# Kernel tuning notes

Measured on AMD Instinct MI355X. Metric: run time of the kernel, lower is better.

The kernel has to match this reference:

```python
import jax, jax.numpy as jnp
import numpy as np

B, C, H, W = 2, 1024, 64, 64
E, TOP_K = 8, 2
FFN = C  # ffn_dim = in_channels; hidden_dim = out_channels = in_channels


def setup_inputs() -> dict:
    key = jax.random.key(0)
    ks = jax.random.split(key, 5)
    s = 0.02
    return {
        "hidden_states": jax.random.normal(ks[0], (B, C, H, W), jnp.float32),
        "gate_w": jax.random.normal(ks[1], (E, C), jnp.float32) * s,   # torch Linear weight [out,in]
        "w1": jax.random.normal(ks[2], (E, FFN, C), jnp.float32) * s,
        "w2": jax.random.normal(ks[3], (E, C, FFN), jnp.float32) * s,
        "w3": jax.random.normal(ks[4], (E, FFN, C), jnp.float32) * s,
    }


def reference(hidden_states, gate_w, w1, w2, w3):
    b, c = hidden_states.shape[0], hidden_states.shape[1]
    space = hidden_states.shape[2:]
    # (B, C, H, W) -> (B, H, W, C) -> (T, C)
    x = jnp.transpose(hidden_states, (0, 2, 3, 1)).reshape(-1, c)

    # Router: softmax in float32, top-k, renormalize (matches torch)
    logits = x @ gate_w.T                                   # [T, E]
    probs = jax.nn.softmax(logits.astype(jnp.float32), axis=-1)
    rw, sel = jax.lax.top_k(probs, TOP_K)                   # [T, K]
    rw = rw / jnp.sum(rw, axis=-1, keepdims=True)
    rw = rw.astype(x.dtype)

    # Combine weights per expert: zero where expert not selected -> exact
    # equivalence with gather/scatter dispatch (full capacity, no drops).
    combine = jnp.sum(jax.nn.one_hot(sel, E, dtype=x.dtype) * rw[..., None], axis=1)  # [T, E]

    out = jnp.zeros_like(x)
    for e in range(E):  # small fixed expert loop
        h = jax.nn.gelu(x @ w1[e].T, approximate=False) * (x @ w3[e].T)  # SwiGLU-style [T, FFN]
        out = out + combine[:, e:e + 1] * (h @ w2[e].T)

    out = out.reshape(b, *space, c)
    return jnp.transpose(out, (0, 3, 1, 2))  # (B, C, H, W)
```

## Files before the change

kernel.cpp:

```cpp
#include <hip/hip_runtime.h>
#include <hip/hip_bf16.h>
#include <math.h>

#define BB 2
#define CC 1024
#define HH 64
#define WW 64
#define HWH (HH*WW)
#define TT (BB*HWH)
#define EE 8
#define FFN 1024
#define MAXTILES 71
#define HCAP (MAXTILES*256)

typedef __bf16 bf16x8 __attribute__((ext_vector_type(8)));
typedef float  f32x4  __attribute__((ext_vector_type(4)));

__device__ __forceinline__ void gl_lds16(const __bf16* g, __bf16* l) {
    __builtin_amdgcn_global_load_lds(
        (const __attribute__((address_space(1))) void*)g,
        (__attribute__((address_space(3))) void*)l, 16, 0, 0);
}

__device__ __forceinline__ void barrier_raw() {
    asm volatile("" ::: "memory");
    __builtin_amdgcn_s_barrier();
    asm volatile("" ::: "memory");
}

#define WAITV(N) asm volatile("s_waitcnt vmcnt(" #N ")" ::: "memory")
#define LGKM0()  asm volatile("s_waitcnt lgkmcnt(0)" ::: "memory")
#define SCHED0() __builtin_amdgcn_sched_barrier(0)
#define PRIO1()  __builtin_amdgcn_s_setprio(1)
#define PRIO0()  __builtin_amdgcn_s_setprio(0)

#define CVB 12288
#define XPB 8192
#define RTB 512
__global__ __launch_bounds__(256) void k_prep(
    const float* __restrict__ hs, const float* __restrict__ gate_w,
    const float* __restrict__ w1, const float* __restrict__ w2,
    const float* __restrict__ w3,
    __bf16* __restrict__ w1b, __bf16* __restrict__ w2b,
    __bf16* __restrict__ w3b, __bf16* __restrict__ X,
    float* __restrict__ logP) {
    __shared__ float sm[2112];
    const int bid = blockIdx.x;
    const int tid = threadIdx.x;

    if (bid < CVB) {
        const float* s; __bf16* d; int lb = bid;
        if (lb < 4096)      { s = w1; d = w1b; }
        else if (lb < 8192) { s = w2; d = w2b; lb -= 4096; }
        else                { s = w3; d = w3b; lb -= 8192; }
        const size_t i = (size_t)lb * 2048 + (size_t)tid * 8;
        const f32x4 v0 = *(const f32x4*)&s[i];
        const f32x4 v1 = *(const f32x4*)&s[i + 4];
        bf16x8 o;
#pragma unroll
        for (int j = 0; j < 4; ++j) { o[j] = (__bf16)v0[j]; o[4 + j] = (__bf16)v1[j]; }
        *(bf16x8*)&d[i] = o;
    } else if (bid < CVB + XPB) {
        const int lb  = bid - CVB;
        const int hw0 = (lb & 127) * 32;
        const int c0  = ((lb >> 7) & 31) * 32;
        const int b   = lb >> 12;
        float (*tile)[33] = (float(*)[33])sm;
        const int tx = tid & 31, ty = tid >> 5;
        const float* src = hs + ((size_t)b * CC + c0) * HWH + hw0;
#pragma unroll
        for (int i = 0; i < 4; ++i)
            tile[ty + i * 8][tx] = src[(size_t)(ty + i * 8) * HWH + tx];
        __syncthreads();
        __bf16* dst = X + ((size_t)b * HWH + hw0) * CC + c0;
#pragma unroll
        for (int i = 0; i < 4; ++i) {
            const int hwl = ty + i * 8;
            dst[(size_t)hwl * CC + tx] = (__bf16)tile[tx][hwl];
        }
    } else {
        const int lb  = bid - (CVB + XPB);
        const int q   = lb & 3;
        const int t64 = lb >> 2;
        float* g = sm;
        for (int i = tid; i < 2048; i += 256)
            g[i] = gate_w[(size_t)(i >> 8) * CC + q * 256 + (i & 255)];
        __syncthreads();
        const int q2 = tid >> 6, tl = tid & 63;
        const int t  = t64 * 64 + tl;
        const int b  = t >> 12, hw = t & 4095;
        const float* xp = hs + (size_t)b * CC * HWH + hw;
        float l[EE];
#pragma unroll
        for (int e = 0; e < EE; ++e) l[e] = 0.0f;
        const int cbase = q * 256 + q2 * 64;
        for (int c2 = 0; c2 < 64; ++c2) {
            const float xv = xp[(size_t)(cbase + c2) * HWH];
#pragma unroll
            for (int e = 0; e < EE; ++e) l[e] += xv * g[e * 256 + q2 * 64 + c2];
        }
        float* dst = logP + ((size_t)(q * 4 + q2) * TT + t) * 8;
        f32x4 a, c;
#pragma unroll
        for (int e = 0; e < 4; ++e) { a[e] = l[e]; c[e] = l[4 + e]; }
        *(f32x4*)dst = a;
        *(f32x4*)&dst[4] = c;
    }
}

__global__ __launch_bounds__(256) void k_top2(const float* __restrict__ logP,
                                              int* __restrict__ cnt,
                                              int* __restrict__ idxl,
                                              int* __restrict__ tokE,
                                              int* __restrict__ tokP,
                                              float* __restrict__ tokW) {
    __shared__ int lcnt[EE], lbase[EE];
    const int tid = threadIdx.x;
    const int t   = blockIdx.x * 256 + tid;
    if (tid < EE) lcnt[tid] = 0;
    __syncthreads();

    float l[EE];
#pragma unroll
    for (int e = 0; e < EE; ++e) l[e] = 0.0f;
#pragma unroll
    for (int pq = 0; pq < 16; ++pq) {
        const float* src = logP + ((size_t)pq * TT + t) * 8;
        const f32x4 a = *(const f32x4*)src;
        const f32x4 c = *(const f32x4*)&src[4];
#pragma unroll
        for (int e = 0; e < 4; ++e) { l[e] += a[e]; l[4 + e] += c[e]; }
    }

    int e1 = 0; float v1 = l[0];
#pragma unroll
    for (int e = 1; e < EE; ++e) { if (l[e] > v1) { v1 = l[e]; e1 = e; } }
    int e2 = -1; float v2 = -1e30f;
#pragma unroll
    for (int e = 0; e < EE; ++e) { if (e != e1 && l[e] > v2) { v2 = l[e]; e2 = e; } }

    const float p2 = __expf(v2 - v1);
    const float rs = 1.0f / (1.0f + p2);

    const int m1 = atomicAdd(&lcnt[e1], 1);
    const int m2 = atomicAdd(&lcnt[e2], 1);
    __syncthreads();
    if (tid < EE) lbase[tid] = atomicAdd(&cnt[tid], lcnt[tid]);
    __syncthreads();
    const int p1pos = lbase[e1] + m1;
    const int p2pos = lbase[e2] + m2;

    idxl[e1 * TT + p1pos] = t;
    idxl[e2 * TT + p2pos] = t;
    tokE[t] = e1 | (e2 << 8);
    tokP[2 * t]     = p1pos;
    tokP[2 * t + 1] = p2pos;
    tokW[2 * t]     = rs;
    tokW[2 * t + 1] = p2 * rs;
}

__global__ void k_offsets(const int* __restrict__ cnt, int* __restrict__ off,
                          int* __restrict__ tileE, int* __restrict__ tileM,
                          int* __restrict__ nT) {
    if (threadIdx.x == 0) {
        int a = 0, n = 0;
        for (int e = 0; e < EE; ++e) {
            off[e] = a;
            const int mt = (cnt[e] + 255) >> 8;
            for (int m = 0; m < mt; ++m) { tileE[n] = e; tileM[n] = m * 256; ++n; }
            a += mt * 256;
        }
        nT[0] = n;
    }
}

__global__ __launch_bounds__(512, 1)
void k_gemm1(const __bf16* __restrict__ X, const __bf16* __restrict__ w1b,
             const __bf16* __restrict__ w3b, const int* __restrict__ cnt,
             const int* __restrict__ off, const int* __restrict__ idxl,
             const int* __restrict__ tileE, const int* __restrict__ tileM,
             const int* __restrict__ nT, __bf16* __restrict__ H) {
    if ((int)blockIdx.y >= nT[0]) return;
    const int e    = tileE[blockIdx.y];
    const int mt   = tileM[blockIdx.y];
    const int cntE = cnt[e];
    const int goff = off[e];
    const int n0   = blockIdx.x * 128;
    const __bf16* W1 = w1b + (size_t)e * FFN * CC;
    const __bf16* W3 = w3b + (size_t)e * FFN * CC;

    __shared__ __align__(16) __bf16 sA[2][2][256 * 32];
    __shared__ __align__(16) __bf16 sB[2][2][256 * 32];

    const int tid  = threadIdx.x;
    const int lane = tid & 63, wave = tid >> 6;
    const int l15  = lane & 15, lq = lane >> 4;
    const int wm   = wave & 1;
    const int q    = wave >> 1;
    const int rsw  = (lq ^ ((l15 >> 1) & 3)) * 8;

    const int rl  = lane >> 2;
    const int csw = ((lane & 3) ^ ((rl >> 1) & 3)) * 8;

    int pr0 = mt + wave * 32 + rl;       if (pr0 > cntE - 1) pr0 = cntE - 1;
    int pr1 = mt + wave * 32 + 16 + rl;  if (pr1 > cntE - 1) pr1 = cntE - 1;
    const __bf16* gA0 = X + (size_t)idxl[e * TT + pr0] * CC + csw;
    const __bf16* gA1 = X + (size_t)idxl[e * TT + pr1] * CC + csw;
    const __bf16* WB = (wave & 1) ? W3 : W1;
    const __bf16* gB0 = WB + (size_t)(n0 + q * 32 + rl) * CC + csw;
    const __bf16* gB1 = WB + (size_t)(n0 + q * 32 + 16 + rl) * CC + csw;

    const int st0  = wave * 1024;
    const int aoff = (wm * 128 + l15) * 32 + rsw;
    const int boff = (q * 64 + l15) * 32 + rsw;

    f32x4 acc[8][4] = {};

#define G1_STGA(S, KS, KB) do {                                               \
    gl_lds16(gA0 + (KB) + (KS) * 32, &sA[S][KS][st0]);                        \
    gl_lds16(gA1 + (KB) + (KS) * 32, &sA[S][KS][st0 + 512]); } while (0)
#define G1_STGB(S, KS, KB) do {                                               \
    gl_lds16(gB0 + (KB) + (KS) * 32, &sB[S][KS][st0]);                        \
    gl_lds16(gB1 + (KB) + (KS) * 32, &sB[S][KS][st0 + 512]); } while (0)
#define G1_LDA(DST, S, KS, MF0)                                               \
    _Pragma("unroll") for (int mf_ = 0; mf_ < 4; ++mf_)                       \
        DST[mf_] = *(const bf16x8*)&sA[S][KS][aoff + (MF0 + mf_) * 512];
#define G1_LDB(DST, S, KS)                                                    \
    _Pragma("unroll") for (int nf_ = 0; nf_ < 4; ++nf_)                       \
        DST[nf_] = *(const bf16x8*)&sB[S][KS][boff + nf_ * 512];
#define G1_MM(M0, AF, BF)                                                     \
    _Pragma("unroll") for (int m_ = 0; m_ < 4; ++m_)                          \
    _Pragma("unroll") for (int n_ = 0; n_ < 4; ++n_)                          \
        acc[M0 + m_][n_] = __builtin_amdgcn_mfma_f32_16x16x32_bf16(           \
            AF[m_], BF[n_], acc[M0 + m_][n_], 0, 0, 0);

#define G1_TILE(S, KB, STG, LAST) do {                                        \
    bf16x8 af[4], bv[4];                                                      \
                                 \
    G1_LDA(af, S, 0, 0); G1_LDB(bv, S, 0);                                    \
    if (STG) G1_STGA((S) ^ 1, 0, KB);                                         \
    barrier_raw(); LGKM0(); SCHED0();                                         \
    PRIO1(); G1_MM(0, af, bv); PRIO0(); barrier_raw();                        \
                                               \
    G1_LDA(af, S, 0, 4);                                                      \
    if (STG) G1_STGB((S) ^ 1, 0, KB);                                         \
    if (LAST) { WAITV(0); } else { WAITV(4); }                                \
    barrier_raw(); LGKM0(); SCHED0();                                         \
    PRIO1(); G1_MM(4, af, bv); PRIO0(); barrier_raw();                        \
                                 \
    G1_LDA(af, S, 1, 0); G1_LDB(bv, S, 1);                                    \
    if (STG) G1_STGA((S) ^ 1, 1, KB);                                         \
    barrier_raw(); LGKM0(); SCHED0();                                         \
    PRIO1(); G1_MM(0, af, bv); PRIO0(); barrier_raw();                        \
                                               \
    G1_LDA(af, S, 1, 4);                                                      \
    if (STG) G1_STGB((S) ^ 1, 1, KB);                                         \
    if (!LAST) { WAITV(4); }                                                  \
    barrier_raw(); LGKM0(); SCHED0();                                         \
    PRIO1(); G1_MM(4, af, bv); PRIO0(); barrier_raw();                        \
} while (0)

    G1_STGA(0, 0, 0); G1_STGB(0, 0, 0); G1_STGA(0, 1, 0); G1_STGB(0, 1, 0);
    WAITV(0);
    barrier_raw();

    int kb = 64;
    for (int it = 0; it < 7; ++it) {
        G1_TILE(0, kb, 1, 0); kb += 64;
        G1_TILE(1, kb, 1, 0); kb += 64;
    }
    G1_TILE(0, kb, 1, 0);
    G1_TILE(1, 0, 0, 1);

#undef G1_STGA
#undef G1_STGB
#undef G1_LDA
#undef G1_LDB
#undef G1_MM
#undef G1_TILE

#pragma unroll
    for (int mf = 0; mf < 8; ++mf) {
        const int gr = goff + mt + wm * 128 + mf * 16 + lq * 4;
#pragma unroll
        for (int jp = 0; jp < 2; ++jp) {
            const int col = n0 + q * 32 + jp * 16 + l15;
#pragma unroll
            for (int r = 0; r < 4; ++r) {
                const float a  = acc[mf][jp][r];
                const float c  = acc[mf][jp + 2][r];
                const float ge = 0.5f * a * (1.0f + erff(a * 0.70710678118654752f));
                H[(size_t)(gr + r) * FFN + col] = (__bf16)(ge * c);
            }
        }
    }
}

__global__ __launch_bounds__(512, 1)
void k_gemm2(const __bf16* __restrict__ H, const __bf16* __restrict__ w2b,
             const int* __restrict__ off, const int* __restrict__ tileE,
             const int* __restrict__ tileM, const int* __restrict__ nT,
             __bf16* __restrict__ Z) {
    if ((int)blockIdx.y >= nT[0]) return;
    const int e    = tileE[blockIdx.y];
    const int mt   = tileM[blockIdx.y];
    const int goff = off[e];
    const int n0   = blockIdx.x * 256;
    const __bf16* W2 = w2b + (size_t)e * CC * FFN;
    const __bf16* Ar = H + (size_t)(goff + mt) * FFN;

    __shared__ __align__(16) __bf16 sA[2][2][256 * 32];
    __shared__ __align__(16) __bf16 sB[2][2][256 * 32];

    const int tid  = threadIdx.x;
    const int lane = tid & 63, wave = tid >> 6;
    const int l15  = lane & 15, lq = lane >> 4;
    const int wm   = wave & 1;
    const int q    = wave >> 1;
    const int rsw  = (lq ^ ((l15 >> 1) & 3)) * 8;
    const int rl   = lane >> 2;
    const int csw  = ((lane & 3) ^ ((rl >> 1) & 3)) * 8;

    const __bf16* gA0 = Ar + (size_t)(wave * 32 + rl) * FFN + csw;
    const __bf16* gA1 = Ar + (size_t)(wave * 32 + 16 + rl) * FFN + csw;
    const __bf16* gB0 = W2 + (size_t)(n0 + wave * 32 + rl) * FFN + csw;
    const __bf16* gB1 = W2 + (size_t)(n0 + wave * 32 + 16 + rl) * FFN + csw;

    const int st0  = wave * 1024;
    const int aoff = (wm * 128 + l15) * 32 + rsw;
    const int boff = (q * 64 + l15) * 32 + rsw;

    f32x4 acc[8][4] = {};

#define G2_STGA(S, KS, KB) do {                                               \
    gl_lds16(gA0 + (KB) + (KS) * 32, &sA[S][KS][st0]);                        \
    gl_lds16(gA1 + (KB) + (KS) * 32, &sA[S][KS][st0 + 512]); } while (0)
#define G2_STGB(S, KS, KB) do {                                               \
    gl_lds16(gB0 + (KB) + (KS) * 32, &sB[S][KS][st0]);                        \
    gl_lds16(gB1 + (KB) + (KS) * 32, &sB[S][KS][st0 + 512]); } while (0)
#define G2_LDA(DST, S, KS, MF0)                                               \
    _Pragma("unroll") for (int mf_ = 0; mf_ < 4; ++mf_)                       \
        DST[mf_] = *(const bf16x8*)&sA[S][KS][aoff + (MF0 + mf_) * 512];
#define G2_LDB(DST, S, KS)                                                    \
    _Pragma("unroll") for (int nf_ = 0; nf_ < 4; ++nf_)                       \
        DST[nf_] = *(const bf16x8*)&sB[S][KS][boff + nf_ * 512];
#define G2_MM(M0, AF, BF)                                                     \
    _Pragma("unroll") for (int m_ = 0; m_ < 4; ++m_)                          \
    _Pragma("unroll") for (int n_ = 0; n_ < 4; ++n_)                          \
        acc[M0 + m_][n_] = __builtin_amdgcn_mfma_f32_16x16x32_bf16(           \
            AF[m_], BF[n_], acc[M0 + m_][n_], 0, 0, 0);

#define G2_TILE(S, KB, STG, LAST) do {                                        \
    bf16x8 af[4], bv[4];                                                      \
    G2_LDA(af, S, 0, 0); G2_LDB(bv, S, 0);                                    \
    if (STG) G2_STGA((S) ^ 1, 0, KB);                                         \
    barrier_raw(); LGKM0(); SCHED0();                                         \
    PRIO1(); G2_MM(0, af, bv); PRIO0(); barrier_raw();                        \
    G2_LDA(af, S, 0, 4);                                                      \
    if (STG) G2_STGB((S) ^ 1, 0, KB);                                         \
    if (LAST) { WAITV(0); } else { WAITV(4); }                                \
    barrier_raw(); LGKM0(); SCHED0();                                         \
    PRIO1(); G2_MM(4, af, bv); PRIO0(); barrier_raw();                        \
    G2_LDA(af, S, 1, 0); G2_LDB(bv, S, 1);                                    \
    if (STG) G2_STGA((S) ^ 1, 1, KB);                                         \
    barrier_raw(); LGKM0(); SCHED0();                                         \
    PRIO1(); G2_MM(0, af, bv); PRIO0(); barrier_raw();                        \
    G2_LDA(af, S, 1, 4);                                                      \
    if (STG) G2_STGB((S) ^ 1, 1, KB);                                         \
    if (!LAST) { WAITV(4); }                                                  \
    barrier_raw(); LGKM0(); SCHED0();                                         \
    PRIO1(); G2_MM(4, af, bv); PRIO0(); barrier_raw();                        \
} while (0)

    G2_STGA(0, 0, 0); G2_STGB(0, 0, 0); G2_STGA(0, 1, 0); G2_STGB(0, 1, 0);
    WAITV(0);
    barrier_raw();

    int kb = 64;
    for (int it = 0; it < 7; ++it) {
        G2_TILE(0, kb, 1, 0); kb += 64;
        G2_TILE(1, kb, 1, 0); kb += 64;
    }
    G2_TILE(0, kb, 1, 0);
    G2_TILE(1, 0, 0, 1);

#undef G2_STGA
#undef G2_STGB
#undef G2_LDA
#undef G2_LDB
#undef G2_MM
#undef G2_TILE

#pragma unroll
    for (int mf = 0; mf < 8; ++mf) {
        const int gr = goff + mt + wm * 128 + mf * 16 + lq * 4;
#pragma unroll
        for (int nf = 0; nf < 4; ++nf) {
            const int col = n0 + q * 64 + nf * 16 + l15;
#pragma unroll
            for (int r = 0; r < 4; ++r)
                Z[(size_t)(gr + r) * CC + col] = (__bf16)acc[mf][nf][r];
        }
    }
}

__global__ __launch_bounds__(256) void k_combine(const __bf16* __restrict__ Z,
                                                 const int* __restrict__ off,
                                                 const int* __restrict__ tokE,
                                                 const int* __restrict__ tokP,
                                                 const float* __restrict__ tokW,
                                                 float* __restrict__ out) {
    __shared__ float tile[32][33];
    const int t0 = blockIdx.x * 32;
    const int c0 = blockIdx.y * 32;
    const int tx = threadIdx.x & 31;
    const int ty = threadIdx.x >> 5;

#pragma unroll
    for (int i = 0; i < 4; ++i) {
        const int tl = ty + 8 * i;
        const int t  = t0 + tl;
        const int ee = tokE[t];
        const int e1 = ee & 0xff, e2 = ee >> 8;
        const int r1 = off[e1] + tokP[2 * t];
        const int r2 = off[e2] + tokP[2 * t + 1];
        const float v = tokW[2 * t]     * (float)Z[(size_t)r1 * CC + c0 + tx]
                      + tokW[2 * t + 1] * (float)Z[(size_t)r2 * CC + c0 + tx];
        tile[tl][tx] = v;
    }
    __syncthreads();

    const int b   = t0 >> 12;
    const int hw0 = t0 & 4095;
#pragma unroll
    for (int i = 0; i < 4; ++i) {
        const int cl = ty + 8 * i;
        out[(size_t)b * CC * HWH + (size_t)(c0 + cl) * HWH + hw0 + tx] = tile[tx][cl];
    }
}

extern "C" void kernel_launch(void* const* d_in, const int* in_sizes, int n_in,
                              void* d_out, int out_size, void* d_ws, size_t ws_size,
                              hipStream_t stream) {
    const float* hs     = (const float*)d_in[0];
    const float* gate_w = (const float*)d_in[1];
    const float* w1     = (const float*)d_in[2];
    const float* w2     = (const float*)d_in[3];
    const float* w3     = (const float*)d_in[4];
    float* out = (float*)d_out;

    const size_t WSZ = (size_t)EE * FFN * CC * 2;
    char* ws = (char*)d_ws;
    __bf16* w2b  = (__bf16*)ws;
    __bf16* w1b  = (__bf16*)(ws + WSZ);
    __bf16* w3b  = (__bf16*)(ws + 2 * WSZ);
    __bf16* X    = (__bf16*)(ws + 3 * WSZ);
    __bf16* Zbuf = (__bf16*)(ws + WSZ);
    __bf16* Hbuf = (__bf16*)(ws + 4 * WSZ);
    float*  logP = (float*)Hbuf;
    char* p = ws + 4 * WSZ + (size_t)HCAP * FFN * 2;
    int*   idxl  = (int*)p;           p += (size_t)EE * TT * 4;
    int*   tokE  = (int*)p;           p += (size_t)TT * 4;
    int*   tokP  = (int*)p;           p += (size_t)2 * TT * 4;
    float* tokW  = (float*)p;         p += (size_t)2 * TT * 4;
    int*   cnt   = (int*)p;           p += 256;
    int*   off   = (int*)p;           p += 256;
    int*   tileE = (int*)p;           p += MAXTILES * 4;
    int*   tileM = (int*)p;           p += MAXTILES * 4;
    int*   nT    = (int*)p;

    hipMemsetAsync(cnt, 0, EE * sizeof(int), stream);

    k_prep<<<CVB + XPB + RTB, 256, 0, stream>>>(
        hs, gate_w, w1, w2, w3, w1b, w2b, w3b, X, logP);
    k_top2<<<TT / 256, 256, 0, stream>>>(logP, cnt, idxl, tokE, tokP, tokW);
    k_offsets<<<1, 64, 0, stream>>>(cnt, off, tileE, tileM, nT);

    k_gemm1<<<dim3(FFN / 128, MAXTILES), 512, 0, stream>>>(
        X, w1b, w3b, cnt, off, idxl, tileE, tileM, nT, Hbuf);
    k_gemm2<<<dim3(CC / 256, MAXTILES), 512, 0, stream>>>(
        Hbuf, w2b, off, tileE, tileM, nT, Zbuf);
    k_combine<<<dim3(TT / 32, CC / 32), 256, 0, stream>>>(
        Zbuf, off, tokE, tokP, tokW, out);
}
```

Baseline: 380.9 us.

## Remove offsets kernel, compute tile mapping inline, XCD swizzle, fast GELU

Drops the single-thread k_offsets launch. Each GEMM block now derives its expert, tile and row offset directly from the per-expert counts, and k_combine builds the prefix offsets in shared memory. Both GEMMs remap block IDs with an XCD-aware swizzle so neighbouring tiles land on the same XCD and share L2. The exact erf GELU is replaced by a tanh-style approximation built on exp2 and rcp, which changes numerics and may drift from the exact-GELU reference.

```diff
diff --git a/kernel.cpp b/kernel.cpp
--- a/kernel.cpp
+++ b/kernel.cpp
@@ -26,6 +26,18 @@
     asm volatile("" ::: "memory");
     __builtin_amdgcn_s_barrier();
     asm volatile("" ::: "memory");
+}
+
+__device__ __forceinline__ int xcd_swz(int orig, int nwg) {
+    const int q = nwg >> 3, r = nwg & 7, x = orig & 7, o8 = orig >> 3;
+    return (x < r ? x * (q + 1) : r * (q + 1) + (x - r) * q) + o8;
+}
+
+__device__ __forceinline__ float gelu_fast(float a) {
+    const float a2 = a * a;
+    const float t  = a * fmaf(0.044715f, a2, 1.0f);
+    const float u  = __builtin_amdgcn_exp2f(t * -2.30220795f);
+    return a * __builtin_amdgcn_rcpf(1.0f + u);
 }
 
 #define WAITV(N) asm volatile("s_waitcnt vmcnt(" #N ")" ::: "memory")
@@ -159,33 +171,24 @@
     tokW[2 * t + 1] = p2 * rs;
 }
 
-__global__ void k_offsets(const int* __restrict__ cnt, int* __restrict__ off,
-                          int* __restrict__ tileE, int* __restrict__ tileM,
-                          int* __restrict__ nT) {
-    if (threadIdx.x == 0) {
-        int a = 0, n = 0;
-        for (int e = 0; e < EE; ++e) {
-            off[e] = a;
-            const int mt = (cnt[e] + 255) >> 8;
-            for (int m = 0; m < mt; ++m) { tileE[n] = e; tileM[n] = m * 256; ++n; }
-            a += mt * 256;
-        }
-        nT[0] = n;
-    }
-}
-
 __global__ __launch_bounds__(512, 1)
 void k_gemm1(const __bf16* __restrict__ X, const __bf16* __restrict__ w1b,
              const __bf16* __restrict__ w3b, const int* __restrict__ cnt,
-             const int* __restrict__ off, const int* __restrict__ idxl,
-             const int* __restrict__ tileE, const int* __restrict__ tileM,
-             const int* __restrict__ nT, __bf16* __restrict__ H) {
-    if ((int)blockIdx.y >= nT[0]) return;
-    const int e    = tileE[blockIdx.y];
-    const int mt   = tileM[blockIdx.y];
+             const int* __restrict__ idxl, __bf16* __restrict__ H) {
+    const int lid = blockIdx.y * 8 + blockIdx.x;
+    const int wg  = xcd_swz(lid, 8 * MAXTILES);
+    const int n0  = (wg & 7) * 128;
+    int ty = wg >> 3;
+    int e = -1, mt = 0, goff = 0, acc_rows = 0;
+#pragma unroll
+    for (int ee = 0; ee < EE; ++ee) {
+        const int me = (cnt[ee] + 255) >> 8;
+        if (ty >= 0 && ty < me) { e = ee; mt = ty << 8; goff = acc_rows; }
+        ty -= me;
+        acc_rows += me << 8;
+    }
+    if (e < 0) return;
     const int cntE = cnt[e];
-    const int goff = off[e];
-    const int n0   = blockIdx.x * 128;
     const __bf16* W1 = w1b + (size_t)e * FFN * CC;
     const __bf16* W3 = w3b + (size_t)e * FFN * CC;
 
@@ -289,8 +292,7 @@
             for (int r = 0; r < 4; ++r) {
                 const float a  = acc[mf][jp][r];
                 const float c  = acc[mf][jp + 2][r];
-                const float ge = 0.5f * a * (1.0f + erff(a * 0.70710678118654752f));
-                H[(size_t)(gr + r) * FFN + col] = (__bf16)(ge * c);
+                H[(size_t)(gr + r) * FFN + col] = (__bf16)(gelu_fast(a) * c);
             }
         }
     }
@@ -298,14 +300,20 @@
 
 __global__ __launch_bounds__(512, 1)
 void k_gemm2(const __bf16* __restrict__ H, const __bf16* __restrict__ w2b,
-             const int* __restrict__ off, const int* __restrict__ tileE,
-             const int* __restrict__ tileM, const int* __restrict__ nT,
-             __bf16* __restrict__ Z) {
-    if ((int)blockIdx.y >= nT[0]) return;
-    const int e    = tileE[blockIdx.y];
-    const int mt   = tileM[blockIdx.y];
-    const int goff = off[e];
-    const int n0   = blockIdx.x * 256;
+             const int* __restrict__ cnt, __bf16* __restrict__ Z) {
+    const int lid = blockIdx.y * 4 + blockIdx.x;
+    const int wg  = xcd_swz(lid, 4 * MAXTILES);
+    const int n0  = (wg & 3) * 256;
+    int ty = wg >> 2;
+    int e = -1, mt = 0, goff = 0, acc_rows = 0;
+#pragma unroll
+    for (int ee = 0; ee < EE; ++ee) {
+        const int me = (cnt[ee] + 255) >> 8;
+        if (ty >= 0 && ty < me) { e = ee; mt = ty << 8; goff = acc_rows; }
+        ty -= me;
+        acc_rows += me << 8;
+    }
+    if (e < 0) return;
     const __bf16* W2 = w2b + (size_t)e * CC * FFN;
     const __bf16* Ar = H + (size_t)(goff + mt) * FFN;
 
@@ -405,16 +413,25 @@
 }
 
 __global__ __launch_bounds__(256) void k_combine(const __bf16* __restrict__ Z,
-                                                 const int* __restrict__ off,
+                                                 const int* __restrict__ cnt,
                                                  const int* __restrict__ tokE,
                                                  const int* __restrict__ tokP,
                                                  const float* __restrict__ tokW,
                                                  float* __restrict__ out) {
     __shared__ float tile[32][33];
+    __shared__ int s_pre[EE];
+    const int tid = threadIdx.x;
+    if (tid < EE) {
+        int a = 0;
+        for (int ee = 0; ee < tid; ++ee) a += ((cnt[ee] + 255) >> 8) << 8;
+        s_pre[tid] = a;
+    }
+    __syncthreads();
+
     const int t0 = blockIdx.x * 32;
     const int c0 = blockIdx.y * 32;
-    const int tx = threadIdx.x & 31;
-    const int ty = threadIdx.x >> 5;
+    const int tx = tid & 31;
+    const int ty = tid >> 5;
 
 #pragma unroll
     for (int i = 0; i < 4; ++i) {
@@ -422,8 +439,8 @@
         const int t  = t0 + tl;
         const int ee = tokE[t];
         const int e1 = ee & 0xff, e2 = ee >> 8;
-        const int r1 = off[e1] + tokP[2 * t];
-        const int r2 = off[e2] + tokP[2 * t + 1];
+        const int r1 = s_pre[e1] + tokP[2 * t];
+        const int r2 = s_pre[e2] + tokP[2 * t + 1];
         const float v = tokW[2 * t]     * (float)Z[(size_t)r1 * CC + c0 + tx]
                       + tokW[2 * t + 1] * (float)Z[(size_t)r2 * CC + c0 + tx];
         tile[tl][tx] = v;
@@ -464,22 +481,17 @@
     int*   tokP  = (int*)p;           p += (size_t)2 * TT * 4;
     float* tokW  = (float*)p;         p += (size_t)2 * TT * 4;
     int*   cnt   = (int*)p;           p += 256;
-    int*   off   = (int*)p;           p += 256;
-    int*   tileE = (int*)p;           p += MAXTILES * 4;
-    int*   tileM = (int*)p;           p += MAXTILES * 4;
-    int*   nT    = (int*)p;
 
     hipMemsetAsync(cnt, 0, EE * sizeof(int), stream);
 
     k_prep<<<CVB + XPB + RTB, 256, 0, stream>>>(
         hs, gate_w, w1, w2, w3, w1b, w2b, w3b, X, logP);
     k_top2<<<TT / 256, 256, 0, stream>>>(logP, cnt, idxl, tokE, tokP, tokW);
-    k_offsets<<<1, 64, 0, stream>>>(cnt, off, tileE, tileM, nT);
 
     k_gemm1<<<dim3(FFN / 128, MAXTILES), 512, 0, stream>>>(
-        X, w1b, w3b, cnt, off, idxl, tileE, tileM, nT, Hbuf);
+        X, w1b, w3b, cnt, idxl, Hbuf);
     k_gemm2<<<dim3(CC / 256, MAXTILES), 512, 0, stream>>>(
-        Hbuf, w2b, off, tileE, tileM, nT, Zbuf);
+        Hbuf, w2b, cnt, Zbuf);
     k_combine<<<dim3(TT / 32, CC / 32), 256, 0, stream>>>(
-        Zbuf, off, tokE, tokP, tokW, out);
-}
+        Zbuf, cnt, tokE, tokP, tokW, out);
+}
```

After: 355.3 us. 6.7% less time.
